# Kernel tuning notes

Hardware: AMD Instinct MI355X
Metric: run time of the kernel (lower is better)

## Reference

```python
import jax, jax.numpy as jnp
import numpy as np

B, N, D = 1, 4096, 512
H, HD = 8, 64
NBINS = 512
CAND = 64
SCALE = 1.0 / np.sqrt(HD)
MAX_NORM = 1.0 - 1e-5
TWO_PI = 2.0 * np.pi


def _project(x):
    # Poincare-ball style projection: clip L2 norm of each point to MAX_NORM.
    n = jnp.sqrt(jnp.sum(x * x, axis=-1, keepdims=True))
    s = jnp.minimum(1.0, MAX_NORM / jnp.maximum(n, 1e-12))
    return x * s


def _bins(x):
    # Deterministic geometric binning (DavisCache stand-in): quantize the
    # angle of the first two coordinates into NBINS bins.
    ang = jnp.arctan2(x[..., 1], x[..., 0])  # (-pi, pi]
    b = jnp.floor((ang / TWO_PI + 0.5) * NBINS)
    return jnp.clip(b, 0, NBINS - 1).astype(jnp.int32)


def setup_inputs() -> dict:
    key0 = jax.random.key(0)
    ks = jax.random.split(key0, 12)
    w = 0.02  # typical init scale for projection weights
    return {
        "query": jax.random.normal(ks[0], (B, N, D), dtype=jnp.float32),
        "key": jax.random.normal(ks[1], (B, N, D), dtype=jnp.float32),
        "value": jax.random.normal(ks[2], (B, N, D), dtype=jnp.float32),
        "Wq": jax.random.normal(ks[3], (D, D), dtype=jnp.float32) * w,
        "bq": jnp.zeros((D,), dtype=jnp.float32),
        "Wk": jax.random.normal(ks[4], (D, D), dtype=jnp.float32) * w,
        "bk": jnp.zeros((D,), dtype=jnp.float32),
        "Wv": jax.random.normal(ks[5], (D, D), dtype=jnp.float32) * w,
        "bv": jnp.zeros((D,), dtype=jnp.float32),
        "Wo": jax.random.normal(ks[6], (D, D), dtype=jnp.float32) * w,
        "bo": jnp.zeros((D,), dtype=jnp.float32),
    }


def reference(query, key, value, Wq, bq, Wk, bk, Wv, bv, Wo, bo):
    Bq, Nq, Dm = query.shape
    Nk = key.shape[1]
    # projections + split heads -> (B, H, N, HD)
    q = (query @ Wq.T + bq).reshape(Bq, Nq, H, HD).transpose(0, 2, 1, 3)
    k = (key @ Wk.T + bk).reshape(Bq, Nk, H, HD).transpose(0, 2, 1, 3)
    v = (value @ Wv.T + bv).reshape(Bq, Nk, H, HD).transpose(0, 2, 1, 3)
    q = _project(q)
    k = _project(k)

    # geometric binning; candidate keys for a query are those whose bin is
    # within radius 1 of the query's bin (neighboring_bins, radius=1).
    qb = _bins(q)  # (B, H, Nq) int32
    kb = _bins(k)  # (B, H, Nk) int32
    mask = jnp.abs(qb[..., :, None] - kb[..., None, :]) <= 1  # (B,H,Nq,Nk)
    # fallback: if a query has no candidates, attend over all keys
    any_valid = jnp.any(mask, axis=-1, keepdims=True)
    eff = jnp.where(any_valid, mask, True)
    # keep only the first CAND candidates per query (by key index)
    rank = jnp.cumsum(eff.astype(jnp.int32), axis=-1) - 1
    sel = eff & (rank < CAND)

    scores = jnp.einsum("bhqd,bhkd->bhqk", q, k) * SCALE
    scores = jnp.where(sel, scores, -jnp.inf)
    attn = jax.nn.softmax(scores, axis=-1)  # dropout p=0.0 (eval mode)
    out = jnp.einsum("bhqk,bhkd->bhqd", attn, v)

    out = out.transpose(0, 2, 1, 3).reshape(Bq, Nq, Dm)
    return out @ Wo.T + bo
```

## Files before the change

### kernel.cpp

```cpp
#include <hip/hip_runtime.h>
#include <math.h>

typedef unsigned short u16;
typedef __attribute__((ext_vector_type(8))) short v8bf;
typedef __attribute__((ext_vector_type(4))) float f32x4;

#define N_TOK 4096
#define DMODEL 512
#define NHEAD 8
#define HDIM 64
#define CANDN 64
#define NBINS 512
#define BINCAP 64
#define QCAP 128
#define ATT_SCALE 0.125f
#define MAX_NORM_F 0.99999f

__device__ __forceinline__ float bf2f(u16 u) {
  union { unsigned int i; float f; } v; v.i = ((unsigned int)u) << 16; return v.f;
}
__device__ __forceinline__ u16 f2bf(float f) {
  union { float f; unsigned int i; } v; v.f = f;
  unsigned int x = v.i;
  return (u16)((x + 0x7fffu + ((x >> 16) & 1u)) >> 16);
}
__device__ __forceinline__ uint4 load_pack8(const float* __restrict__ p) {
  const float4 x0 = *(const float4*)p;
  const float4 x1 = *(const float4*)(p + 4);
  union { u16 h[8]; uint4 u; } r;
  r.h[0] = f2bf(x0.x); r.h[1] = f2bf(x0.y); r.h[2] = f2bf(x0.z); r.h[3] = f2bf(x0.w);
  r.h[4] = f2bf(x1.x); r.h[5] = f2bf(x1.y); r.h[6] = f2bf(x1.z); r.h[7] = f2bf(x1.w);
  return r.u;
}

__global__ __launch_bounds__(256) void prep_kernel(
    const float* __restrict__ query, const float* __restrict__ key_,
    const float* __restrict__ value,
    const float* __restrict__ Wq, const float* __restrict__ Wk,
    const float* __restrict__ Wv, const float* __restrict__ Wo,
    u16* __restrict__ qx, u16* __restrict__ kx, u16* __restrict__ vx,
    u16* __restrict__ wqx, u16* __restrict__ wkx, u16* __restrict__ wvx,
    u16* __restrict__ wox,
    int* __restrict__ qb, int* __restrict__ kb, unsigned char* __restrict__ flags)
{
  __shared__ float xs[16 * 516];
  const int blk = blockIdx.x;
  const int tid = threadIdx.x;

  if (blk >= 512) {
    const int rel = blk - 512;
    const float* src; u16* dst; int base;
    if (rel < 1024)      { src = query; dst = qx; base = rel << 11; }
    else if (rel < 2048) { src = key_;  dst = kx; base = (rel - 1024) << 11; }
    else if (rel < 3072) { src = value; dst = vx; base = (rel - 2048) << 11; }
    else {
      const int r2 = rel - 3072; const int w = r2 >> 7;
      src = (w == 0) ? Wq : (w == 1) ? Wk : (w == 2) ? Wv : Wo;
      dst = (w == 0) ? wqx : (w == 1) ? wkx : (w == 2) ? wvx : wox;
      base = (r2 & 127) << 11;
    }
    const int off = base + tid * 8;
    *(uint4*)(dst + off) = load_pack8(src + off);
    return;
  }

  const int isk  = blk >> 8;
  const int tile = blk & 255;
  const float* X = isk ? key_ : query;
  const float* W = isk ? Wk : Wq;

#pragma unroll
  for (int i = 0; i < 8; ++i) {
    const int flat = i * 1024 + tid * 4;
    const int row = flat >> 9, col = flat & 511;
    *(float4*)&xs[row * 516 + col] = *(const float4*)(X + (tile * 16 + row) * DMODEL + col);
  }
  __syncthreads();

  const int n_local = tid >> 4;
  const int pair = tid & 15;
  const int h = pair >> 1, coord = pair & 1;
  const float* wrow = W + ((h << 6) + coord) * DMODEL;
  const float* xrow = &xs[n_local * 516];

  double c0 = 0.0, c1 = 0.0, c2 = 0.0, c3 = 0.0;
  for (int k = 0; k < DMODEL; k += 4) {
    const float4 xv = *(const float4*)(xrow + k);
    const float4 wv = *(const float4*)(wrow + k);
    c0 = fma((double)xv.x, (double)wv.x, c0);
    c1 = fma((double)xv.y, (double)wv.y, c1);
    c2 = fma((double)xv.z, (double)wv.z, c2);
    c3 = fma((double)xv.w, (double)wv.w, c3);
  }
  const double a = (c0 + c1) + (c2 + c3);
  const double other = __shfl_xor(a, 1);
  if (coord == 0) {
    const double a0 = a, a1 = other;
    const int n = tile * 16 + n_local;
    double ang = atan2(a1, a0);
    double t = (ang / 6.283185307179586 + 0.5) * 512.0;
    int b = (int)floor(t);
    b = b < 0 ? 0 : (b > 511 ? 511 : b);
    (isk ? kb : qb)[(h << 12) + n] = b;

    const double r = sqrt(a0 * a0 + a1 * a1);
    const double dist = fabs(t - nearbyint(t));
    const double margin = fmin(0.45, 3.3e-4 / fmax(r, 1e-30) + 5e-5);
    flags[(isk << 15) | (h << 12) | n] = (dist < margin) ? 1 : 0;
  }
}

__device__ float fdlibm_atanf(float x) {
#pragma clang fp contract(off)
  const float atanhi[4] = {4.6364760399e-01f, 7.8539812565e-01f,
                           9.8279368877e-01f, 1.5707962513e+00f};
  const float atanlo[4] = {5.0121582440e-09f, 3.7748947079e-08f,
                           3.4473217170e-08f, 7.5497894159e-08f};
  const float aT[5] = {3.3333328366e-01f, -1.9999158382e-01f, 1.4253635705e-01f,
                       -1.0648017377e-01f, 6.1687607318e-02f};
  unsigned ix = __float_as_uint(x);
  const unsigned sign = ix >> 31;
  ix &= 0x7fffffffu;
  int id;
  float z, w, s1, s2;
  if (ix >= 0x4c800000u) {
    z = atanhi[3] + 0x1p-120f;
    return sign ? -z : z;
  }
  if (ix < 0x3ee00000u) {
    if (ix < 0x39800000u) return x;
    id = -1;
  } else {
    x = fabsf(x);
    if (ix < 0x3f980000u) {
      if (ix < 0x3f300000u) { id = 0; x = (2.0f * x - 1.0f) / (2.0f + x); }
      else                  { id = 1; x = (x - 1.0f) / (x + 1.0f); }
    } else {
      if (ix < 0x401c0000u) { id = 2; x = (x - 1.5f) / (1.0f + 1.5f * x); }
      else                  { id = 3; x = -1.0f / x; }
    }
  }
  z = x * x;
  w = z * z;
  s1 = z * (aT[0] + w * (aT[2] + w * aT[4]));
  s2 = w * (aT[1] + w * aT[3]);
  if (id < 0) return x - x * (s1 + s2);
  z = atanhi[id] - ((x * (s1 + s2) - atanlo[id]) - x);
  return sign ? -z : z;
}

__device__ float fdlibm_atan2f(float y, float x) {
#pragma clang fp contract(off)
  const float pi = 3.1415927410e+00f, pi_lo = -8.7422776573e-08f;
  const unsigned hx = __float_as_uint(x), hy = __float_as_uint(y);
  if (hx == 0x3f800000u) return fdlibm_atanf(y);
  const unsigned m = ((hy >> 31) & 1u) | ((hx >> 30) & 2u);
  const unsigned ix = hx & 0x7fffffffu, iy = hy & 0x7fffffffu;
  if (iy == 0u) {
    switch (m) { case 0: case 1: return y; case 2: return pi; default: return -pi; }
  }
  if (ix == 0u) return (m & 1u) ? -1.57079637050628662f : 1.57079637050628662f;
  float z;
  if (ix + (26u << 23) < iy) {
    z = 1.57079637050628662f;
    return (m & 1u) ? -z : z;
  }
  if ((m & 2u) && iy + (26u << 23) < ix) z = 0.0f;
  else z = fdlibm_atanf(fabsf(y / x));
  switch (m) {
    case 0: return z;
    case 1: return -z;
    case 2: return pi - (z - pi_lo);
    default: return (z - pi_lo) - pi;
  }
}

__global__ __launch_bounds__(256) void gemmfix_kernel(
    const u16* __restrict__ qx, const u16* __restrict__ kx, const u16* __restrict__ vx,
    const u16* __restrict__ wqx, const u16* __restrict__ wkx, const u16* __restrict__ wvx,
    const float* __restrict__ bq, const float* __restrict__ bk, const float* __restrict__ bv,
    const float* __restrict__ query, const float* __restrict__ key_,
    const float* __restrict__ Wq, const float* __restrict__ Wk,
    const unsigned char* __restrict__ flags,
    int* __restrict__ qb, int* __restrict__ kb,
    u16* __restrict__ Qb, u16* __restrict__ Kb, u16* __restrict__ Vb)
{
  __shared__ u16 As[128 * 40];
  __shared__ u16 Ws[128 * 40];
  __shared__ int wle[64];
  __shared__ int wlc;

  const int blk = blockIdx.x;
  const int tid = threadIdx.x;

  if (blk >= 384) {
    const int slice = blk - 384;
    if (tid == 0) wlc = 0;
    __syncthreads();
    for (int i = tid; i < 1024; i += 256) {
      const int flat = slice * 1024 + i;
      if (flags[flat]) {
        const int p = atomicAdd(&wlc, 1);
        if (p < 64) wle[p] = flat;
      }
    }
    __syncthreads();
    int nw = wlc; if (nw > 64) nw = 64;
    const int w = tid >> 6, d = tid & 63;
    for (int e = w; e < nw; e += 4) {
      const int flat = wle[e];
      const int n = flat & 4095;
      const int h = (flat >> 12) & 7;
      const int isk = flat >> 15;
      const float* xr = (isk ? key_ : query) + n * DMODEL;
      const float* wr = (isk ? Wk : Wq) + ((h << 6) + d) * DMODEL;
      float acc = 0.0f;
      for (int k = 0; k < DMODEL; k += 16) {
        const float4 xa = *(const float4*)(xr + k);
        const float4 xb = *(const float4*)(xr + k + 4);
        const float4 xc = *(const float4*)(xr + k + 8);
        const float4 xd = *(const float4*)(xr + k + 12);
        const float4 wa = *(const float4*)(wr + k);
        const float4 wb = *(const float4*)(wr + k + 4);
        const float4 wc = *(const float4*)(wr + k + 8);
        const float4 wd = *(const float4*)(wr + k + 12);
        acc = __fmaf_rn(xa.x, wa.x, acc); acc = __fmaf_rn(xa.y, wa.y, acc);
        acc = __fmaf_rn(xa.z, wa.z, acc); acc = __fmaf_rn(xa.w, wa.w, acc);
        acc = __fmaf_rn(xb.x, wb.x, acc); acc = __fmaf_rn(xb.y, wb.y, acc);
        acc = __fmaf_rn(xb.z, wb.z, acc); acc = __fmaf_rn(xb.w, wb.w, acc);
        acc = __fmaf_rn(xc.x, wc.x, acc); acc = __fmaf_rn(xc.y, wc.y, acc);
        acc = __fmaf_rn(xc.z, wc.z, acc); acc = __fmaf_rn(xc.w, wc.w, acc);
        acc = __fmaf_rn(xd.x, wd.x, acc); acc = __fmaf_rn(xd.y, wd.y, acc);
        acc = __fmaf_rn(xd.z, wd.z, acc); acc = __fmaf_rn(xd.w, wd.w, acc);
      }
      {
#pragma clang fp contract(off)
        const float sq = acc * acc;
        float rr[8];
#pragma unroll
        for (int j = 0; j < 8; ++j) rr[j] = __shfl(sq, j);
        for (int i = 8; i < 64; i += 8) {
#pragma unroll
          for (int j = 0; j < 8; ++j) rr[j] += __shfl(sq, i + j);
        }
        const float ss = ((rr[0] + rr[1]) + (rr[2] + rr[3])) +
                         ((rr[4] + rr[5]) + (rr[6] + rr[7]));
        const float nrm = __fsqrt_rn(ss);
        const float s = fminf(1.0f, 0.99999f / fmaxf(nrm, 1e-12f));
        const float c0 = __shfl(acc, 0) * s;
        const float c1 = __shfl(acc, 1) * s;
        const float cr = (float)atan2((double)c1, (double)c0);
        const float fd = fdlibm_atan2f(c1, c0);
        const float tol = fmaxf(fabsf(cr) * 6e-7f, 1e-30f);
        const float ang = (fabsf(fd - cr) <= tol) ? fd : cr;
        const float t = ((ang / 6.2831854820251465f) + 0.5f) * 512.0f;
        int b = (int)floorf(t);
        b = b < 0 ? 0 : (b > 511 ? 511 : b);
        if (d == 0) (isk ? kb : qb)[(h << 12) + n] = b;
      }
    }
    return;
  }

  const int z = blk >> 7;
  const int rem = blk & 127;
  const int bm = (rem & 31) * 128;
  const int bn = (rem >> 5) * 128;

  const u16* A    = (z == 0) ? qx : (z == 1) ? kx : vx;
  const u16* W    = (z == 0) ? wqx : (z == 1) ? wkx : wvx;
  const float* bias = (z == 0) ? bq : (z == 1) ? bk : bv;
  u16* O          = (z == 0) ? Qb : (z == 1) ? Kb : Vb;

  const int lane = tid & 63;
  const int wave = tid >> 6;
  const int row4 = tid >> 2;
  const int seg  = tid & 3;
  const int wm = (wave & 1) * 64;
  const int wn = (wave >> 1) * 64;
  const int l15 = lane & 15;
  const int quad = lane >> 4;

  f32x4 acc[4][4] = {};

  for (int kt = 0; kt < DMODEL; kt += 32) {
    uint4 a0 = *(const uint4*)(A + (bm + row4) * DMODEL + kt + seg * 8);
    uint4 a1 = *(const uint4*)(A + (bm + row4 + 64) * DMODEL + kt + seg * 8);
    uint4 w0 = *(const uint4*)(W + (bn + row4) * DMODEL + kt + seg * 8);
    uint4 w1 = *(const uint4*)(W + (bn + row4 + 64) * DMODEL + kt + seg * 8);
    __syncthreads();
    *(uint4*)&As[row4 * 40 + seg * 8] = a0;
    *(uint4*)&As[(row4 + 64) * 40 + seg * 8] = a1;
    *(uint4*)&Ws[row4 * 40 + seg * 8] = w0;
    *(uint4*)&Ws[(row4 + 64) * 40 + seg * 8] = w1;
    __syncthreads();
    v8bf af[4], bfr[4];
#pragma unroll
    for (int i = 0; i < 4; ++i)
      af[i] = *(const v8bf*)&As[(wm + i * 16 + l15) * 40 + quad * 8];
#pragma unroll
    for (int j = 0; j < 4; ++j)
      bfr[j] = *(const v8bf*)&Ws[(wn + j * 16 + l15) * 40 + quad * 8];
#pragma unroll
    for (int i = 0; i < 4; ++i)
#pragma unroll
      for (int j = 0; j < 4; ++j)
        acc[i][j] = __builtin_amdgcn_mfma_f32_16x16x32_bf16(af[i], bfr[j], acc[i][j], 0, 0, 0);
  }

  float bval[4];
#pragma unroll
  for (int j = 0; j < 4; ++j) bval[j] = bias[bn + wn + j * 16 + l15];
  const int h = (bn + wn) >> 6;

#pragma unroll
  for (int i = 0; i < 4; ++i) {
#pragma unroll
    for (int r = 0; r < 4; ++r) {
      const int row = bm + wm + i * 16 + quad * 4 + r;
      float v0 = acc[i][0][r] + bval[0];
      float v1 = acc[i][1][r] + bval[1];
      float v2 = acc[i][2][r] + bval[2];
      float v3 = acc[i][3][r] + bval[3];
      if (z != 2) {
        float ss = v0 * v0 + v1 * v1 + v2 * v2 + v3 * v3;
#pragma unroll
        for (int o = 1; o < 16; o <<= 1) ss += __shfl_xor(ss, o);
        const float s = fminf(1.0f, MAX_NORM_F / fmaxf(sqrtf(ss), 1e-12f));
        v0 *= s; v1 *= s; v2 *= s; v3 *= s;
      }
      const int base = (((h << 12) + row) << 6) + l15;
      O[base +  0] = f2bf(v0); O[base + 16] = f2bf(v1);
      O[base + 32] = f2bf(v2); O[base + 48] = f2bf(v3);
    }
  }
}

__global__ __launch_bounds__(256) void bin_hist_kernel(
    const int* __restrict__ kb, const int* __restrict__ qb,
    int* __restrict__ khist, u16* __restrict__ blist,
    int* __restrict__ qhist, u16* __restrict__ qlist)
{
  const int h = blockIdx.x;
  const int type = blockIdx.y;
  const int* src = type ? qb : kb;
  int* hist = type ? qhist : khist;
  u16* list = type ? qlist : blist;
  const int cap = type ? QCAP : BINCAP;

  __shared__ int lhist[NBINS];
  for (int i = threadIdx.x; i < NBINS; i += 256) lhist[i] = 0;
  __syncthreads();
  for (int i = threadIdx.x; i < N_TOK; i += 256) {
    const int b = src[(h << 12) + i];
    const int pos = atomicAdd(&lhist[b], 1);
    if (pos < cap) list[((h << 9) + b) * cap + pos] = (u16)i;
  }
  __syncthreads();
  for (int i = threadIdx.x; i < NBINS; i += 256)
    hist[(h << 9) + i] = lhist[i] < cap ? lhist[i] : cap;
}

__global__ __launch_bounds__(64) void attn_bin_kernel(
    const u16* __restrict__ Qb, const u16* __restrict__ Kb,
    const u16* __restrict__ Vb, const int* __restrict__ qhist,
    const u16* __restrict__ qlist, const int* __restrict__ khist,
    const u16* __restrict__ blist, u16* __restrict__ aout)
{
  __shared__ u16 kf[4 * 2 * 4 * 16 * 8];
  __shared__ u16 vf[4 * 2 * 4 * 16 * 8];
  __shared__ u16 pf[16 * 72];
  __shared__ u16 s_cand[64];
  __shared__ int s_qg[16];

  const int hb = blockIdx.x;
  const int h = hb >> 9;
  const int b = hb & 511;
  const int qcnt = qhist[hb];
  if (qcnt == 0) return;

  const int lane = threadIdx.x;
  const int l15 = lane & 15;
  const int quad = lane >> 4;

  int v0 = 0xFFFF, v1 = 0xFFFF, v2 = 0xFFFF;
  int c0 = 0, c1 = 0, c2 = 0;
  if (b > 0) {
    c0 = khist[(h << 9) + b - 1];
    if (lane < c0) v0 = (int)blist[(((h << 9) + b - 1) << 6) + lane];
  }
  {
    c1 = khist[(h << 9) + b];
    if (lane < c1) v1 = (int)blist[(((h << 9) + b) << 6) + lane];
  }
  if (b < NBINS - 1) {
    c2 = khist[(h << 9) + b + 1];
    if (lane < c2) v2 = (int)blist[(((h << 9) + b + 1) << 6) + lane];
  }

  int r0 = 0, r1 = 0, r2 = 0;
#pragma unroll 8
  for (int j = 0; j < 64; ++j) {
    const int w0 = __shfl(v0, j);
    const int w1 = __shfl(v1, j);
    const int w2 = __shfl(v2, j);
    r0 += (w0 < v0) + (w1 < v0) + (w2 < v0);
    r1 += (w0 < v1) + (w1 < v1) + (w2 < v1);
    r2 += (w0 < v2) + (w1 < v2) + (w2 < v2);
  }
  const int tot = c0 + c1 + c2;
  const int ccnt = tot < CANDN ? tot : CANDN;
  const int ccnt_eff = (tot == 0) ? 64 : ccnt;
  if (tot == 0) {
    s_cand[lane] = (u16)lane;
  } else {
    if (v0 != 0xFFFF && r0 < CANDN) s_cand[r0] = (u16)v0;
    if (v1 != 0xFFFF && r1 < CANDN) s_cand[r1] = (u16)v1;
    if (v2 != 0xFFFF && r2 < CANDN) s_cand[r2] = (u16)v2;
  }
  __syncthreads();
  if (tot > 0 && lane >= ccnt) s_cand[lane] = s_cand[0];
  __syncthreads();

  {
    const int r = lane >> 3, s = lane & 7;
    const int ks = s >> 2, qd = s & 3;
#pragma unroll
    for (int it = 0; it < 8; ++it) {
      const int key = it * 8 + r;
      const int c = s_cand[key];
      const uint4 kv = *(const uint4*)(Kb + ((h << 18) | (c << 6)) + s * 8);
      const int idx = ((((key >> 4) * 2 + ks) * 4 + qd) * 16 + (key & 15)) * 8;
      *(uint4*)&kf[idx] = kv;
    }
  }
  {
    const int r = lane >> 3, s = lane & 7;
    const int nt = s >> 1, d0 = (s & 1) * 8;
#pragma unroll
    for (int it = 0; it < 8; ++it) {
      const int key = it * 8 + r;
      const int c = s_cand[key];
      union { u16 hh[8]; uint4 u; } vv;
      vv.u = *(const uint4*)(Vb + ((h << 18) | (c << 6)) + s * 8);
      const int kstep = key >> 5, qd = (key >> 3) & 3, j = key & 7;
#pragma unroll
      for (int m = 0; m < 8; ++m)
        vf[(((nt * 2 + kstep) * 4 + qd) * 16 + d0 + m) * 8 + j] = vv.hh[m];
    }
  }
  __syncthreads();

  v8bf akf[4][2], bvf[4][2];
#pragma unroll
  for (int t = 0; t < 4; ++t)
#pragma unroll
    for (int ks = 0; ks < 2; ++ks) {
      akf[t][ks] = *(const v8bf*)&kf[(((t * 2 + ks) * 4 + quad) * 16 + l15) * 8];
      bvf[t][ks] = *(const v8bf*)&vf[(((t * 2 + ks) * 4 + quad) * 16 + l15) * 8];
    }

  const int nchunk = (qcnt + 15) >> 4;
  for (int ci = 0; ci < nchunk; ++ci) {
    const int base = ci << 4;
    const int qcn = min(16, qcnt - base);
    __syncthreads();
    if (lane < 16) {
      int idx = base + lane;
      if (idx > qcnt - 1) idx = qcnt - 1;
      s_qg[lane] = (int)qlist[(hb << 7) + idx];
    }
    __syncthreads();

    const u16* qrow = Qb + ((h << 18) | (s_qg[l15] << 6));
    v8bf bq[2];
#pragma unroll
    for (int ks = 0; ks < 2; ++ks)
      bq[ks] = *(const v8bf*)(qrow + ks * 32 + quad * 8);

    float sc[16];
#pragma unroll
    for (int t = 0; t < 4; ++t) {
      f32x4 sa = {0.f, 0.f, 0.f, 0.f};
      sa = __builtin_amdgcn_mfma_f32_16x16x32_bf16(akf[t][0], bq[0], sa, 0, 0, 0);
      sa = __builtin_amdgcn_mfma_f32_16x16x32_bf16(akf[t][1], bq[1], sa, 0, 0, 0);
#pragma unroll
      for (int r = 0; r < 4; ++r) {
        const int key = t * 16 + quad * 4 + r;
        sc[t * 4 + r] = (key < ccnt_eff) ? sa[r] * ATT_SCALE : -INFINITY;
      }
    }
    float mx = sc[0];
#pragma unroll
    for (int i = 1; i < 16; ++i) mx = fmaxf(mx, sc[i]);
    mx = fmaxf(mx, __shfl_xor(mx, 16));
    mx = fmaxf(mx, __shfl_xor(mx, 32));
    float sum = 0.0f;
    float pe[16];
#pragma unroll
    for (int i = 0; i < 16; ++i) { pe[i] = __expf(sc[i] - mx); sum += pe[i]; }
    sum += __shfl_xor(sum, 16);
    sum += __shfl_xor(sum, 32);
    const float inv = 1.0f / sum;

    __syncthreads();
#pragma unroll
    for (int t = 0; t < 4; ++t)
#pragma unroll
      for (int r = 0; r < 4; ++r)
        pf[l15 * 72 + t * 16 + quad * 4 + r] = f2bf(pe[t * 4 + r] * inv);
    __syncthreads();

    v8bf ap[2];
#pragma unroll
    for (int ks = 0; ks < 2; ++ks)
      ap[ks] = *(const v8bf*)&pf[l15 * 72 + ks * 32 + quad * 8];

#pragma unroll
    for (int nt = 0; nt < 4; ++nt) {
      f32x4 o = {0.f, 0.f, 0.f, 0.f};
      o = __builtin_amdgcn_mfma_f32_16x16x32_bf16(ap[0], bvf[nt][0], o, 0, 0, 0);
      o = __builtin_amdgcn_mfma_f32_16x16x32_bf16(ap[1], bvf[nt][1], o, 0, 0, 0);
#pragma unroll
      for (int r = 0; r < 4; ++r) {
        const int row = quad * 4 + r;
        if (row < qcn)
          aout[s_qg[row] * DMODEL + (h << 6) + nt * 16 + l15] = f2bf(o[r]);
      }
    }
  }
}

__global__ __launch_bounds__(256) void gemm_out_kernel(
    const u16* __restrict__ A, const u16* __restrict__ W,
    const float* __restrict__ bias, float* __restrict__ O)
{
  __shared__ u16 As[128 * 40];
  __shared__ u16 Ws[128 * 40];

  const int tid  = threadIdx.x;
  const int lane = tid & 63;
  const int wave = tid >> 6;
  const int row4 = tid >> 2;
  const int seg  = tid & 3;

  const int bm = blockIdx.x * 128;
  const int bn = blockIdx.y * 128;
  const int wm = (wave & 1) * 64;
  const int wn = (wave >> 1) * 64;
  const int l15 = lane & 15;
  const int quad = lane >> 4;

  f32x4 acc[4][4] = {};

  for (int kt = 0; kt < DMODEL; kt += 32) {
    uint4 a0 = *(const uint4*)(A + (bm + row4) * DMODEL + kt + seg * 8);
    uint4 a1 = *(const uint4*)(A + (bm + row4 + 64) * DMODEL + kt + seg * 8);
    uint4 w0 = *(const uint4*)(W + (bn + row4) * DMODEL + kt + seg * 8);
    uint4 w1 = *(const uint4*)(W + (bn + row4 + 64) * DMODEL + kt + seg * 8);
    __syncthreads();
    *(uint4*)&As[row4 * 40 + seg * 8] = a0;
    *(uint4*)&As[(row4 + 64) * 40 + seg * 8] = a1;
    *(uint4*)&Ws[row4 * 40 + seg * 8] = w0;
    *(uint4*)&Ws[(row4 + 64) * 40 + seg * 8] = w1;
    __syncthreads();
    v8bf af[4], bfr[4];
#pragma unroll
    for (int i = 0; i < 4; ++i)
      af[i] = *(const v8bf*)&As[(wm + i * 16 + l15) * 40 + quad * 8];
#pragma unroll
    for (int j = 0; j < 4; ++j)
      bfr[j] = *(const v8bf*)&Ws[(wn + j * 16 + l15) * 40 + quad * 8];
#pragma unroll
    for (int i = 0; i < 4; ++i)
#pragma unroll
      for (int j = 0; j < 4; ++j)
        acc[i][j] = __builtin_amdgcn_mfma_f32_16x16x32_bf16(af[i], bfr[j], acc[i][j], 0, 0, 0);
  }

#pragma unroll
  for (int j = 0; j < 4; ++j) {
    const int cg = bn + wn + j * 16 + l15;
    const float bval = bias[cg];
#pragma unroll
    for (int i = 0; i < 4; ++i) {
      const int rbase = bm + wm + i * 16 + quad * 4;
#pragma unroll
      for (int r = 0; r < 4; ++r)
        O[(rbase + r) * DMODEL + cg] = acc[i][j][r] + bval;
    }
  }
}

extern "C" void kernel_launch(void* const* d_in, const int* in_sizes, int n_in,
                              void* d_out, int out_size, void* d_ws, size_t ws_size,
                              hipStream_t stream) {
  const float* query = (const float*)d_in[0];
  const float* key_  = (const float*)d_in[1];
  const float* value = (const float*)d_in[2];
  const float* Wq = (const float*)d_in[3];
  const float* bq = (const float*)d_in[4];
  const float* Wk = (const float*)d_in[5];
  const float* bk = (const float*)d_in[6];
  const float* Wv = (const float*)d_in[7];
  const float* bv = (const float*)d_in[8];
  const float* Wo = (const float*)d_in[9];
  const float* bo = (const float*)d_in[10];

  char* ws = (char*)d_ws;
  u16* qx    = (u16*)(ws);
  u16* kx    = (u16*)(ws + 4194304);
  u16* vx    = (u16*)(ws + 8388608);
  u16* wqx   = (u16*)(ws + 12582912);
  u16* wkx   = (u16*)(ws + 13107200);
  u16* wvx   = (u16*)(ws + 13631488);
  u16* wox   = (u16*)(ws + 14155776);
  u16* Qb    = (u16*)(ws + 14680064);
  u16* Kb    = (u16*)(ws + 18874368);
  u16* Vb    = (u16*)(ws + 23068672);
  u16* aout  = (u16*)(ws + 27262976);
  int* qb    = (int*)(ws + 31457280);
  int* kb    = (int*)(ws + 31588352);
  unsigned char* flags = (unsigned char*)(ws + 31719424);
  int* khist = (int*)(ws + 31784960);
  int* qhist = (int*)(ws + 31801344);
  u16* blist = (u16*)(ws + 31817728);
  u16* qlist = (u16*)(ws + 32342016);

  prep_kernel<<<4096, 256, 0, stream>>>(
      query, key_, value, Wq, Wk, Wv, Wo,
      qx, kx, vx, wqx, wkx, wvx, wox, qb, kb, flags);
  gemmfix_kernel<<<448, 256, 0, stream>>>(
      qx, kx, vx, wqx, wkx, wvx, bq, bk, bv,
      query, key_, Wq, Wk, flags, qb, kb, Qb, Kb, Vb);
  bin_hist_kernel<<<dim3(8, 2), 256, 0, stream>>>(
      kb, qb, khist, blist, qhist, qlist);
  attn_bin_kernel<<<4096, 64, 0, stream>>>(
      Qb, Kb, Vb, qhist, qlist, khist, blist, aout);
  gemm_out_kernel<<<dim3(32, 4), 256, 0, stream>>>(aout, wox, bo, (float*)d_out);
}
```

Measured before the change: 208.1 us.

## Use direct global-to-LDS loads in GEMMs and parallelize bin histogram with global atomics

Both bf16 GEMM kernels now stage A and W tiles with global_load_lds instead of loading into registers and then storing to shared memory. The padded LDS row stride of 40 is dropped to an unpadded 32, which may add bank conflicts on the fragment reads. The bin histogram kernel is spread over many blocks that do one token per thread with global atomics, instead of 16 blocks looping over 4096 tokens each. The histograms are zeroed by extra blocks added to the prep kernel. Counts can now exceed the list capacity, so the attention kernel clamps them.

```diff
diff --git a/kernel.cpp b/kernel.cpp
--- a/kernel.cpp
+++ b/kernel.cpp
@@ -33,6 +33,12 @@
   return r.u;
 }
 
+__device__ __forceinline__ void gload16(const u16* __restrict__ g, u16* l) {
+  __builtin_amdgcn_global_load_lds(
+      (const __attribute__((address_space(1))) void*)g,
+      (__attribute__((address_space(3))) void*)l, 16, 0, 0);
+}
+
 __global__ __launch_bounds__(256) void prep_kernel(
     const float* __restrict__ query, const float* __restrict__ key_,
     const float* __restrict__ value,
@@ -41,11 +47,18 @@
     u16* __restrict__ qx, u16* __restrict__ kx, u16* __restrict__ vx,
     u16* __restrict__ wqx, u16* __restrict__ wkx, u16* __restrict__ wvx,
     u16* __restrict__ wox,
-    int* __restrict__ qb, int* __restrict__ kb, unsigned char* __restrict__ flags)
+    int* __restrict__ qb, int* __restrict__ kb, unsigned char* __restrict__ flags,
+    int* __restrict__ khist)
 {
   __shared__ float xs[16 * 516];
   const int blk = blockIdx.x;
   const int tid = threadIdx.x;
+
+  if (blk >= 4096) {
+    int4 z4; z4.x = 0; z4.y = 0; z4.z = 0; z4.w = 0;
+    ((int4*)khist)[((blk - 4096) << 8) + tid] = z4;
+    return;
+  }
 
   if (blk >= 512) {
     const int rel = blk - 512;
@@ -185,8 +198,8 @@
     int* __restrict__ qb, int* __restrict__ kb,
     u16* __restrict__ Qb, u16* __restrict__ Kb, u16* __restrict__ Vb)
 {
-  __shared__ u16 As[128 * 40];
-  __shared__ u16 Ws[128 * 40];
+  __shared__ u16 As[128 * 32];
+  __shared__ u16 Ws[128 * 32];
   __shared__ int wle[64];
   __shared__ int wlc;
 
@@ -274,33 +287,32 @@
 
   const int lane = tid & 63;
   const int wave = tid >> 6;
-  const int row4 = tid >> 2;
-  const int seg  = tid & 3;
   const int wm = (wave & 1) * 64;
   const int wn = (wave >> 1) * 64;
   const int l15 = lane & 15;
   const int quad = lane >> 4;
 
+  const int ca = tid;
+  const int cb = tid + 256;
+  const int ra = ca >> 2, oa = (ca & 3) * 8;
+  const int rb = cb >> 2, ob = (cb & 3) * 8;
+
   f32x4 acc[4][4] = {};
 
   for (int kt = 0; kt < DMODEL; kt += 32) {
-    uint4 a0 = *(const uint4*)(A + (bm + row4) * DMODEL + kt + seg * 8);
-    uint4 a1 = *(const uint4*)(A + (bm + row4 + 64) * DMODEL + kt + seg * 8);
-    uint4 w0 = *(const uint4*)(W + (bn + row4) * DMODEL + kt + seg * 8);
-    uint4 w1 = *(const uint4*)(W + (bn + row4 + 64) * DMODEL + kt + seg * 8);
-    __syncthreads();
-    *(uint4*)&As[row4 * 40 + seg * 8] = a0;
-    *(uint4*)&As[(row4 + 64) * 40 + seg * 8] = a1;
-    *(uint4*)&Ws[row4 * 40 + seg * 8] = w0;
-    *(uint4*)&Ws[(row4 + 64) * 40 + seg * 8] = w1;
+    __syncthreads();
+    gload16(A + (bm + ra) * DMODEL + kt + oa, &As[ca * 8]);
+    gload16(A + (bm + rb) * DMODEL + kt + ob, &As[cb * 8]);
+    gload16(W + (bn + ra) * DMODEL + kt + oa, &Ws[ca * 8]);
+    gload16(W + (bn + rb) * DMODEL + kt + ob, &Ws[cb * 8]);
     __syncthreads();
     v8bf af[4], bfr[4];
 #pragma unroll
     for (int i = 0; i < 4; ++i)
-      af[i] = *(const v8bf*)&As[(wm + i * 16 + l15) * 40 + quad * 8];
+      af[i] = *(const v8bf*)&As[(wm + i * 16 + l15) * 32 + quad * 8];
 #pragma unroll
     for (int j = 0; j < 4; ++j)
-      bfr[j] = *(const v8bf*)&Ws[(wn + j * 16 + l15) * 40 + quad * 8];
+      bfr[j] = *(const v8bf*)&Ws[(wn + j * 16 + l15) * 32 + quad * 8];
 #pragma unroll
     for (int i = 0; i < 4; ++i)
 #pragma unroll
@@ -348,17 +360,10 @@
   u16* list = type ? qlist : blist;
   const int cap = type ? QCAP : BINCAP;
 
-  __shared__ int lhist[NBINS];
-  for (int i = threadIdx.x; i < NBINS; i += 256) lhist[i] = 0;
-  __syncthreads();
-  for (int i = threadIdx.x; i < N_TOK; i += 256) {
-    const int b = src[(h << 12) + i];
-    const int pos = atomicAdd(&lhist[b], 1);
-    if (pos < cap) list[((h << 9) + b) * cap + pos] = (u16)i;
-  }
-  __syncthreads();
-  for (int i = threadIdx.x; i < NBINS; i += 256)
-    hist[(h << 9) + i] = lhist[i] < cap ? lhist[i] : cap;
+  const int i = blockIdx.z * 256 + threadIdx.x;
+  const int b = src[(h << 12) + i];
+  const int pos = atomicAdd(&hist[(h << 9) + b], 1);
+  if (pos < cap) list[((h << 9) + b) * cap + pos] = (u16)i;
 }
 
 __global__ __launch_bounds__(64) void attn_bin_kernel(
@@ -376,7 +381,8 @@
   const int hb = blockIdx.x;
   const int h = hb >> 9;
   const int b = hb & 511;
-  const int qcnt = qhist[hb];
+  int qcnt = qhist[hb];
+  if (qcnt > QCAP) qcnt = QCAP;
   if (qcnt == 0) return;
 
   const int lane = threadIdx.x;
@@ -387,14 +393,17 @@
   int c0 = 0, c1 = 0, c2 = 0;
   if (b > 0) {
     c0 = khist[(h << 9) + b - 1];
+    if (c0 > BINCAP) c0 = BINCAP;
     if (lane < c0) v0 = (int)blist[(((h << 9) + b - 1) << 6) + lane];
   }
   {
     c1 = khist[(h << 9) + b];
+    if (c1 > BINCAP) c1 = BINCAP;
     if (lane < c1) v1 = (int)blist[(((h << 9) + b) << 6) + lane];
   }
   if (b < NBINS - 1) {
     c2 = khist[(h << 9) + b + 1];
+    if (c2 > BINCAP) c2 = BINCAP;
     if (lane < c2) v2 = (int)blist[(((h << 9) + b + 1) << 6) + lane];
   }
 
@@ -535,14 +544,12 @@
     const u16* __restrict__ A, const u16* __restrict__ W,
     const float* __restrict__ bias, float* __restrict__ O)
 {
-  __shared__ u16 As[128 * 40];
-  __shared__ u16 Ws[128 * 40];
+  __shared__ u16 As[128 * 32];
+  __shared__ u16 Ws[128 * 32];
 
   const int tid  = threadIdx.x;
   const int lane = tid & 63;
   const int wave = tid >> 6;
-  const int row4 = tid >> 2;
-  const int seg  = tid & 3;
 
   const int bm = blockIdx.x * 128;
   const int bn = blockIdx.y * 128;
@@ -551,26 +558,27 @@
   const int l15 = lane & 15;
   const int quad = lane >> 4;
 
+  const int ca = tid;
+  const int cb = tid + 256;
+  const int ra = ca >> 2, oa = (ca & 3) * 8;
+  const int rb = cb >> 2, ob = (cb & 3) * 8;
+
   f32x4 acc[4][4] = {};
 
   for (int kt = 0; kt < DMODEL; kt += 32) {
-    uint4 a0 = *(const uint4*)(A + (bm + row4) * DMODEL + kt + seg * 8);
-    uint4 a1 = *(const uint4*)(A + (bm + row4 + 64) * DMODEL + kt + seg * 8);
-    uint4 w0 = *(const uint4*)(W + (bn + row4) * DMODEL + kt + seg * 8);
-    uint4 w1 = *(const uint4*)(W + (bn + row4 + 64) * DMODEL + kt + seg * 8);
-    __syncthreads();
-    *(uint4*)&As[row4 * 40 + seg * 8] = a0;
-    *(uint4*)&As[(row4 + 64) * 40 + seg * 8] = a1;
-    *(uint4*)&Ws[row4 * 40 + seg * 8] = w0;
-    *(uint4*)&Ws[(row4 + 64) * 40 + seg * 8] = w1;
+    __syncthreads();
+    gload16(A + (bm + ra) * DMODEL + kt + oa, &As[ca * 8]);
+    gload16(A + (bm + rb) * DMODEL + kt + ob, &As[cb * 8]);
+    gload16(W + (bn + ra) * DMODEL + kt + oa, &Ws[ca * 8]);
+    gload16(W + (bn + rb) * DMODEL + kt + ob, &Ws[cb * 8]);
     __syncthreads();
     v8bf af[4], bfr[4];
 #pragma unroll
     for (int i = 0; i < 4; ++i)
-      af[i] = *(const v8bf*)&As[(wm + i * 16 + l15) * 40 + quad * 8];
+      af[i] = *(const v8bf*)&As[(wm + i * 16 + l15) * 32 + quad * 8];
 #pragma unroll
     for (int j = 0; j < 4; ++j)
-      bfr[j] = *(const v8bf*)&Ws[(wn + j * 16 + l15) * 40 + quad * 8];
+      bfr[j] = *(const v8bf*)&Ws[(wn + j * 16 + l15) * 32 + quad * 8];
 #pragma unroll
     for (int i = 0; i < 4; ++i)
 #pragma unroll
@@ -627,13 +635,13 @@
   u16* blist = (u16*)(ws + 31817728);
   u16* qlist = (u16*)(ws + 32342016);
 
-  prep_kernel<<<4096, 256, 0, stream>>>(
+  prep_kernel<<<4104, 256, 0, stream>>>(
       query, key_, value, Wq, Wk, Wv, Wo,
-      qx, kx, vx, wqx, wkx, wvx, wox, qb, kb, flags);
+      qx, kx, vx, wqx, wkx, wvx, wox, qb, kb, flags, khist);
   gemmfix_kernel<<<448, 256, 0, stream>>>(
       qx, kx, vx, wqx, wkx, wvx, bq, bk, bv,
       query, key_, Wq, Wk, flags, qb, kb, Qb, Kb, Vb);
-  bin_hist_kernel<<<dim3(8, 2), 256, 0, stream>>>(
+  bin_hist_kernel<<<dim3(8, 2, 16), 256, 0, stream>>>(
       kb, qb, khist, blist, qhist, qlist);
   attn_bin_kernel<<<4096, 64, 0, stream>>>(
       Qb, Kb, Vb, qhist, qlist, khist, blist, aout);
```

Result: slower. 212.6 us (+2.2%).
